# Kernel tuning notes

Measured on AMD Instinct MI355X. Metric: run time of the kernel, lower is better.

Reference implementation:

```python
import jax, jax.numpy as jnp
import numpy as np

B, T, H, C = 16, 6000, 256, 105
NOTE_BD_TEMP = 1.0
THRESH = 0.5
MIN_GAP = 19      # round(100 * 24000 / 1000 / 128)
REF_GAP = 9       # round(50 * 24000 / 1000 / 128)


def setup_inputs() -> dict:
    key = jax.random.key(0)
    kf, kw = jax.random.split(key)
    feat = jax.random.normal(kf, (B, T, H), dtype=jnp.float32)
    # kaiming normal fan_in: std = sqrt(2/fan_in)
    W = jax.random.normal(kw, (C, H), dtype=jnp.float32) * np.float32(np.sqrt(2.0 / H))
    b = jnp.zeros((C,), dtype=jnp.float32)
    rng = np.random.default_rng(0)
    word_bd = np.zeros((B, T), dtype=np.int32)
    for i in range(B):
        pos = np.cumsum(rng.integers(25, 61, size=T // 25)) + 10
        pos = pos[pos < T - 2]
        word_bd[i, pos] = 1
    lengths = rng.integers(T // 2, T + 1, size=B)
    non_padding = (np.arange(T)[None, :] < lengths[:, None]).astype(np.float32)
    return {"feat": feat, "word_bd": jnp.asarray(word_bd),
            "non_padding": jnp.asarray(non_padding), "W": W, "b": b}


def _phase1(probs, bd):
    # Peak-picking + min-gap merging scan over one sequence.
    # probs, bd: [T]. Returns res: [T+1] int32 (slot T is a dummy write sink).
    def step(carry, inp):
        res, last, start, rmv, rmi = carry
        j, bj, pj = inp
        in_run = start >= 0
        upd = (~in_run) | (pj > rmv)          # running first-argmax of current run
        fin = (~bj) & in_run                  # run just ended at j
        bd_idx = rmi                          # argmax index of the run (== start if len 1)
        merge = fin & (bd_idx - last < MIN_GAP) & (last > 0)
        mid = jnp.round((bd_idx + last).astype(jnp.float32) / 2.0).astype(jnp.int32)
        bd_idx = jnp.where(merge, mid, bd_idx)
        res = res.at[jnp.where(merge, last, T)].set(0)
        res = res.at[jnp.where(fin, bd_idx, T)].set(1)
        last = jnp.where(fin, bd_idx, last)
        start = jnp.where(bj, jnp.where(in_run, start, j), jnp.where(fin, -1, start))
        rmv = jnp.where(bj & upd, pj, rmv)
        rmi = jnp.where(bj & upd, j, rmi)
        return (res, last, start, rmv, rmi), None

    init = (jnp.zeros((T + 1,), jnp.int32), jnp.int32(-1), jnp.int32(-1),
            jnp.float32(-1e30), jnp.int32(0))
    xs = (jnp.arange(T, dtype=jnp.int32), bd, probs)
    (res, _, _, _, _), _ = jax.lax.scan(step, init, xs)
    return res


def _phase2(res, ref):
    # Reconcile predicted boundaries with reference word boundaries.
    ds = jnp.arange(-REF_GAP, REF_GAP)        # window [j-g, j+g-1] == torch slice [j-g : j+g]
    ks = jnp.arange(1, REF_GAP + 1)

    def step(res, j):
        active = ref[j] == 1
        widx = j + ds
        valid = (widx >= 0) & (widx < T)
        cwidx = jnp.clip(widx, 0, T - 1)
        seg = jnp.sum(jnp.where(valid, res[cwidx], 0))
        b0 = seg == 0
        b1 = (seg == 1) & (res[j] != 1)
        b2 = seg > 1
        # branch seg>1: first (in l1,r1,l2,r2,... order) offending boundary to suppress
        lidx = jnp.maximum(0, j - ks)
        ridx = jnp.minimum(T - 1, j + ks)
        cl = (res[lidx] == 1) & (ref[lidx] != 1)
        cr = (res[ridx] == 1) & (ref[ridx] != 1)
        conds = jnp.stack([cl, cr], axis=1).reshape(-1)
        cands = jnp.stack([lidx, ridx], axis=1).reshape(-1)
        zidx = jnp.where(jnp.any(conds), cands[jnp.argmax(conds)], T)
        # apply branch effects (inactive writes go to dummy slot T)
        res = res.at[jnp.where(active & b1 & valid, widx, T)].set(ref[cwidx])
        res = res.at[jnp.where(active & b2, zidx, T)].set(0)
        res = res.at[jnp.where(active & (b0 | b2), j, T)].set(1)
        return res, None

    res, _ = jax.lax.scan(step, res, jnp.arange(T, dtype=jnp.int32))
    return res


def regulate_boundary(bd_logits, word_bd, non_padding):
    probs = jax.nn.sigmoid(bd_logits)
    bd = probs > THRESH
    res = jax.vmap(_phase1)(probs, bd)
    res = jax.vmap(_phase2)(res, word_bd)
    res = res[:, :T]                      # drop dummy slot
    res = res.at[:, 0].set(0)
    L = jnp.sum(non_padding, axis=1).astype(jnp.int32)   # [B]
    keep = jnp.arange(T)[None, :] < (L[:, None] - 1)     # zero out res[i, L-1:]
    return jnp.where(keep, res, 0)


def reference(feat, word_bd, non_padding, W, b):
    # note_head: Linear(H -> C); eval mode so dropout is identity
    logits = jnp.einsum('bth,ch->btc', feat, W) + b           # [B,T,C]
    note_bd_logits = jnp.clip(logits[:, :, 0] / NOTE_BD_TEMP, -16.0, 16.0)
    note_frame_logits = logits[:, :, 1:] / NOTE_BD_TEMP
    note_bd_pred = regulate_boundary(note_bd_logits, word_bd, non_padding)
    return note_bd_logits, note_frame_logits, note_bd_pred
```

## Files before the change

kernel.cpp:

```cpp
#include <hip/hip_runtime.h>

#define NB 16
#define TT 6000
#define HH 256
#define CC 105
#define MIN_GAP_ 19
#define REF_GAP_ 9

using short8  = __attribute__((ext_vector_type(8))) short;
using short4v = __attribute__((ext_vector_type(4))) short;
using f32x4   = __attribute__((ext_vector_type(4))) float;

static __device__ __forceinline__ short f2bf(float x) {
  unsigned u = __builtin_bit_cast(unsigned, x);
  unsigned r = (u + 0x7FFFu + ((u >> 16) & 1u)) >> 16;
  return (short)r;
}

__global__ __launch_bounds__(256) void wconv_kernel(
    const float* __restrict__ W, unsigned short* __restrict__ Wb) {
  const int idx = blockIdx.x * 256 + threadIdx.x;
  const int c = idx >> 8, k = idx & 255;
  const float v = (c < CC - 1) ? W[(size_t)(c + 1) * HH + k] : 0.f;
  Wb[idx] = (unsigned short)f2bf(v);
}

#define BMR 128

__global__ __launch_bounds__(512, 4) void gemm_mfma(
    const float* __restrict__ feat, const float* __restrict__ W,
    const float* __restrict__ bias, const unsigned short* __restrict__ Wb,
    float* __restrict__ out0, float* __restrict__ out1) {
  __shared__ __align__(16) unsigned short aS[BMR * 256];
  const int tid  = threadIdx.x;
  const int wid  = tid >> 6;
  const int lane = tid & 63;
  const int rl   = lane & 15;
  const int kg   = lane >> 4;
  const int row0 = blockIdx.x * BMR;

  float4 areg[16];
  {
    const float* fbase = feat + (size_t)(row0 + wid) * HH + lane * 4;
#pragma unroll
    for (int p = 0; p < 16; p++)
      areg[p] = *reinterpret_cast<const float4*>(fbase + (size_t)p * 8 * HH);
  }

  short8 breg[8];
  if (wid < 7) {
    const unsigned short* wbbase = Wb + ((size_t)(wid * 16 + rl) << 8) + kg * 8;
#pragma unroll
    for (int ks = 0; ks < 8; ks++)
      breg[ks] = *reinterpret_cast<const short8*>(wbbase + ks * 32);
  }

  const float4 w0 = *reinterpret_cast<const float4*>(W + lane * 4);
  const float b0 = bias[0];
#pragma unroll
  for (int p = 0; p < 16; p++) {
    const int lrow = p * 8 + wid;
    const float4 a = areg[p];
    float s = a.x * w0.x;
    s = fmaf(a.y, w0.y, s); s = fmaf(a.z, w0.z, s); s = fmaf(a.w, w0.w, s);
#pragma unroll
    for (int off = 1; off < 64; off <<= 1) s += __shfl_xor(s, off);
    if (lane == 0)
      out0[row0 + lrow] = fminf(fmaxf(s + b0, -16.f), 16.f);
    short4v bf;
    bf[0] = f2bf(a.x); bf[1] = f2bf(a.y); bf[2] = f2bf(a.z); bf[3] = f2bf(a.w);
    const int dst = (lrow << 9) + ((lane * 8) ^ ((lrow & 7) << 4));
    *reinterpret_cast<short4v*>((char*)aS + dst) = bf;
  }
  __syncthreads();

  if (wid < 7) {
    const int xr = (rl & 7) << 4;
    f32x4 acc[8];
#pragma unroll
    for (int rg = 0; rg < 8; rg++) acc[rg] = (f32x4){0.f, 0.f, 0.f, 0.f};

#pragma unroll
    for (int ks = 0; ks < 8; ks++) {
      const int slot = (ks * 64 + kg * 16) ^ xr;
#pragma unroll
      for (int rg = 0; rg < 8; rg++) {
        const short8 av = *reinterpret_cast<const short8*>(
            (const char*)aS + (((rg * 16 + rl) << 9) + slot));
        acc[rg] = __builtin_amdgcn_mfma_f32_16x16x32_bf16(av, breg[ks], acc[rg], 0, 0, 0);
      }
    }

    const int c = wid * 16 + rl;
    if (c < CC - 1) {
      const float bb = bias[c + 1];
#pragma unroll
      for (int rg = 0; rg < 8; rg++) {
        const int rbase = row0 + rg * 16 + kg * 4;
#pragma unroll
        for (int r = 0; r < 4; r++)
          out1[(size_t)(rbase + r) * (CC - 1) + c] = acc[rg][r] + bb;
      }
    }
  }
}

#define NW 192
#define NW_LAST 187
#define CHUNK 32
#define NCLS 19
#define MAXRUNS 3072
#define MAXCH 96

__global__ __launch_bounds__(512) void phase_kernel(
    const float* __restrict__ bd_logits,
    const int* __restrict__ word_bd,
    const float* __restrict__ non_padding,
    float* __restrict__ out2) {
  __shared__ __align__(16) float lbuf[TT];
  __shared__ unsigned char wbuf[TT];
  __shared__ int res[TT];
  __shared__ unsigned bdbits[NW];
  __shared__ int runIdx[MAXRUNS];
  __shared__ int outLast[MAXCH][NCLS + 1];
  __shared__ int chP0[MAXCH];
  __shared__ int inL[MAXCH + 1];
  __shared__ int wsum[8];
  __shared__ int wbase[8];
  __shared__ int L_sh, nruns_sh;

  const int b = blockIdx.x;
  const int tid = threadIdx.x;
  const int lane = tid & 63;
  const int wid = tid >> 6;
  if (tid == 0) L_sh = 0;
  __syncthreads();

  int cnt_np = 0;
#pragma unroll
  for (int k = 0; k < 12; k++) {
    const int j = k * 512 + tid;
    bool pred = false;
    if (j < TT) {
      const float l = bd_logits[(size_t)b * TT + j];
      lbuf[j] = l;
      pred = l > 0.f;
      wbuf[j] = (unsigned char)word_bd[(size_t)b * TT + j];
      res[j] = 0;
      cnt_np += (non_padding[(size_t)b * TT + j] != 0.f) ? 1 : 0;
    }
    const unsigned long long m = __ballot(pred);
    if (lane == 0) {
      const int w0 = (k * 512 + (tid & ~63)) >> 5;
      bdbits[w0]     = (unsigned)m;
      bdbits[w0 + 1] = (unsigned)(m >> 32);
    }
  }
#pragma unroll
  for (int off = 32; off; off >>= 1) cnt_np += __shfl_xor(cnt_np, off);
  if (lane == 0) atomicAdd(&L_sh, cnt_np);
  __syncthreads();

  int cnt = 0;
  unsigned ends = 0;
  if (tid < NW) {
    const unsigned cur = bdbits[tid];
    const unsigned pb = tid ? (bdbits[tid - 1] >> 31) : 0u;
    ends = ((cur << 1) | pb) & ~cur;
    if (tid == NW_LAST) ends &= 0xFFFFu;
    cnt = __popc(ends);
  }
  int v = cnt;
#pragma unroll
  for (int off = 1; off < 64; off <<= 1) {
    const int t = __shfl_up(v, off);
    if (lane >= off) v += t;
  }
  if (lane == 63) wsum[wid] = v;
  __syncthreads();
  if (tid == 0) {
    int s = 0;
#pragma unroll
    for (int w = 0; w < 8; w++) { wbase[w] = s; s += wsum[w]; }
    nruns_sh = s;
  }
  __syncthreads();
  int slot = wbase[wid] + v - cnt;

  if (ends) {
    unsigned m = ends;
    while (m) {
      const int bit = __builtin_ctz(m);
      m &= m - 1;
      const int e = tid * 32 + bit;
      const int eb = e - 1;
      int w = eb >> 5;
      const int bb = eb & 31;
      const unsigned z = bdbits[w] << (31 - bb);
      const unsigned nz = ~z;
      int run = nz ? __builtin_clz(nz) : 32;
      if (run == bb + 1) {
        while (w > 0) {
          w--;
          const unsigned nx = ~bdbits[w];
          const int t2 = nx ? __builtin_clz(nx) : 32;
          run += t2;
          if (t2 < 32) break;
        }
      }
      const int s = e - run;
      float mv = lbuf[s];
      int mi = s;
      for (int i = s + 1; i < e; i++) {
        const float val = lbuf[i];
        if (val > mv) { mv = val; mi = i; }
      }
      runIdx[slot++] = mi;
    }
  }
  __syncthreads();

  const int n = nruns_sh;
  const int nch = (n + CHUNK - 1) / CHUNK;
  for (int f = tid; f < nch * NCLS; f += 512) {
    const int ch = f / NCLS;
    const int cls = f - ch * NCLS;
    const int s = ch * CHUNK;
    const int e = (s + CHUNK < n) ? s + CHUNK : n;
    const int p0 = runIdx[s];
    if (cls == NCLS - 1) chP0[ch] = p0;
    int last = (cls < 18) ? (p0 - 18 + cls) : -1;
    for (int i = s; i < e; i++) {
      int bd = runIdx[i];
      if (last > 0 && bd - last < MIN_GAP_) {
        const int sum = bd + last;
        const int h = sum >> 1;
        bd = (sum & 1) ? (h + (h & 1)) : h;
      }
      last = bd;
    }
    outLast[ch][cls] = last;
  }
  __syncthreads();

  if (wid == 0) {
    int q = -1;
    int row = (lane < NCLS && nch > 0) ? outLast[0][lane] : -1;
    for (int ch = 0; ch < nch; ch++) {
      const int rown = (lane < NCLS && ch + 1 < nch) ? outLast[ch + 1][lane] : -1;
      const int p0 = chP0[ch];
      const int cls = (q > 0 && p0 - q < MIN_GAP_) ? (q - (p0 - 18)) : (NCLS - 1);
      if (lane == 0) inL[ch] = q;
      q = __shfl(row, cls);
      row = rown;
    }
    if (lane == 0) inL[nch] = q;
  }
  __syncthreads();

  for (int ch = tid; ch < nch; ch += 512) {
    const int s = ch * CHUNK;
    const int e = (s + CHUNK < n) ? s + CHUNK : n;
    const int qin = inL[ch];
    const int qout = inL[ch + 1];
    if (qin >= 0 && qin != qout) res[qin] = 1;
    int last = qin;
    for (int i = s; i < e; i++) {
      int bd = runIdx[i];
      if (last > 0 && bd - last < MIN_GAP_) {
        const int sum = bd + last;
        const int h = sum >> 1;
        bd = (sum & 1) ? (h + (h & 1)) : h;
        if (last != qout) res[last] = 0;
      }
      if (bd != qout) res[bd] = 1;
      last = bd;
    }
  }
  if (tid == 0 && n > 0) res[inL[nch]] = 1;
  __syncthreads();

  for (int j = tid; j < TT; j += 512) {
    if (wbuf[j] != 1) continue;
    const int lo = (j - REF_GAP_ < 0) ? 0 : j - REF_GAP_;
    const int hi = (j + REF_GAP_ - 1 > TT - 1) ? TT - 1 : j + REF_GAP_ - 1;
    int seg = 0;
    for (int w = lo; w <= hi; w++) seg += res[w];
    if (seg == 0) {
      res[j] = 1;
    } else if (seg == 1) {
      if (res[j] != 1) {
        for (int w = lo; w <= hi; w++) res[w] = (int)wbuf[w];
      }
    } else {
      int zidx = -1;
      for (int k = 1; k <= REF_GAP_; k++) {
        const int li = (j - k < 0) ? 0 : j - k;
        const int ri = (j + k > TT - 1) ? TT - 1 : j + k;
        if (res[li] == 1 && wbuf[li] != 1) { zidx = li; break; }
        if (res[ri] == 1 && wbuf[ri] != 1) { zidx = ri; break; }
      }
      if (zidx >= 0) res[zidx] = 0;
      res[j] = 1;
    }
  }
  __syncthreads();

  const int L = L_sh;
  for (int t = tid; t < TT; t += 512)
    out2[(size_t)b * TT + t] = (t >= 1 && t < L - 1) ? (float)res[t] : 0.f;
}

extern "C" void kernel_launch(void* const* d_in, const int* in_sizes, int n_in,
                              void* d_out, int out_size, void* d_ws, size_t ws_size,
                              hipStream_t stream) {
  const float* feat        = (const float*)d_in[0];
  const int*   word_bd     = (const int*)d_in[1];
  const float* non_padding = (const float*)d_in[2];
  const float* W           = (const float*)d_in[3];
  const float* bias        = (const float*)d_in[4];

  float* out  = (float*)d_out;
  float* out0 = out;
  float* out1 = out + (size_t)NB * TT;
  float* out2 = out + (size_t)NB * TT + (size_t)NB * TT * (CC - 1);

  unsigned short* Wb = (unsigned short*)d_ws;

  hipLaunchKernelGGL(wconv_kernel, dim3(112), dim3(256), 0, stream, W, Wb);
  hipLaunchKernelGGL(gemm_mfma, dim3((NB * TT) / BMR), dim3(512), 0, stream,
                     feat, W, bias, Wb, out0, out1);
  hipLaunchKernelGGL(phase_kernel, dim3(NB), dim3(512), 0, stream,
                     out0, word_bd, non_padding, out2);
}
```

Before: 73.99 us.

## Make GEMM blocks persistent over three 64-row tiles with double-buffered LDS

The GEMM now launches 500 blocks, each handling three 64-row tiles instead of one 128-row tile per block. LDS is double-buffered, and the global feature loads for the next tile are issued before the MFMA and store work on the current tile. The aim is to hide global load latency behind compute and to reuse the B-fragment registers across tiles. In exchange there are fewer blocks, so parallelism drops, and register pressure may rise.

```diff
diff --git a/kernel.cpp b/kernel.cpp
--- a/kernel.cpp
+++ b/kernel.cpp
@@ -25,27 +25,21 @@
   Wb[idx] = (unsigned short)f2bf(v);
 }
 
-#define BMR 128
+#define BMT 64
+#define TPB 3
+#define NGB 500
 
 __global__ __launch_bounds__(512, 4) void gemm_mfma(
     const float* __restrict__ feat, const float* __restrict__ W,
     const float* __restrict__ bias, const unsigned short* __restrict__ Wb,
     float* __restrict__ out0, float* __restrict__ out1) {
-  __shared__ __align__(16) unsigned short aS[BMR * 256];
+  __shared__ __align__(16) unsigned short aS[2][BMT * 256];
   const int tid  = threadIdx.x;
   const int wid  = tid >> 6;
   const int lane = tid & 63;
   const int rl   = lane & 15;
   const int kg   = lane >> 4;
-  const int row0 = blockIdx.x * BMR;
-
-  float4 areg[16];
-  {
-    const float* fbase = feat + (size_t)(row0 + wid) * HH + lane * 4;
-#pragma unroll
-    for (int p = 0; p < 16; p++)
-      areg[p] = *reinterpret_cast<const float4*>(fbase + (size_t)p * 8 * HH);
-  }
+  const int brow0 = blockIdx.x * (BMT * TPB);
 
   short8 breg[8];
   if (wid < 7) {
@@ -57,50 +51,75 @@
 
   const float4 w0 = *reinterpret_cast<const float4*>(W + lane * 4);
   const float b0 = bias[0];
-#pragma unroll
-  for (int p = 0; p < 16; p++) {
-    const int lrow = p * 8 + wid;
-    const float4 a = areg[p];
-    float s = a.x * w0.x;
-    s = fmaf(a.y, w0.y, s); s = fmaf(a.z, w0.z, s); s = fmaf(a.w, w0.w, s);
-#pragma unroll
-    for (int off = 1; off < 64; off <<= 1) s += __shfl_xor(s, off);
-    if (lane == 0)
-      out0[row0 + lrow] = fminf(fmaxf(s + b0, -16.f), 16.f);
-    short4v bf;
-    bf[0] = f2bf(a.x); bf[1] = f2bf(a.y); bf[2] = f2bf(a.z); bf[3] = f2bf(a.w);
-    const int dst = (lrow << 9) + ((lane * 8) ^ ((lrow & 7) << 4));
-    *reinterpret_cast<short4v*>((char*)aS + dst) = bf;
-  }
-  __syncthreads();
-
-  if (wid < 7) {
-    const int xr = (rl & 7) << 4;
-    f32x4 acc[8];
-#pragma unroll
-    for (int rg = 0; rg < 8; rg++) acc[rg] = (f32x4){0.f, 0.f, 0.f, 0.f};
-
-#pragma unroll
-    for (int ks = 0; ks < 8; ks++) {
-      const int slot = (ks * 64 + kg * 16) ^ xr;
-#pragma unroll
-      for (int rg = 0; rg < 8; rg++) {
-        const short8 av = *reinterpret_cast<const short8*>(
-            (const char*)aS + (((rg * 16 + rl) << 9) + slot));
-        acc[rg] = __builtin_amdgcn_mfma_f32_16x16x32_bf16(av, breg[ks], acc[rg], 0, 0, 0);
-      }
-    }
-
-    const int c = wid * 16 + rl;
-    if (c < CC - 1) {
-      const float bb = bias[c + 1];
-#pragma unroll
-      for (int rg = 0; rg < 8; rg++) {
-        const int rbase = row0 + rg * 16 + kg * 4;
-#pragma unroll
-        for (int r = 0; r < 4; r++)
-          out1[(size_t)(rbase + r) * (CC - 1) + c] = acc[rg][r] + bb;
-      }
+  const int cch = wid * 16 + rl;
+  const float bb = (wid < 7 && cch < CC - 1) ? bias[cch + 1] : 0.f;
+  const int xr = (rl & 7) << 4;
+
+  float4 areg[8];
+
+  auto loadA = [&](int trow0) {
+    const float* fbase = feat + (size_t)(trow0 + wid) * HH + lane * 4;
+#pragma unroll
+    for (int q = 0; q < 8; q++)
+      areg[q] = *reinterpret_cast<const float4*>(fbase + (size_t)q * 8 * HH);
+  };
+
+  auto stage = [&](int buf, int trow0) {
+#pragma unroll
+    for (int q = 0; q < 8; q++) {
+      const int lrow = q * 8 + wid;
+      const float4 a = areg[q];
+      float s = a.x * w0.x;
+      s = fmaf(a.y, w0.y, s); s = fmaf(a.z, w0.z, s); s = fmaf(a.w, w0.w, s);
+#pragma unroll
+      for (int off = 1; off < 64; off <<= 1) s += __shfl_xor(s, off);
+      if (lane == 0)
+        out0[trow0 + lrow] = fminf(fmaxf(s + b0, -16.f), 16.f);
+      short4v bf;
+      bf[0] = f2bf(a.x); bf[1] = f2bf(a.y); bf[2] = f2bf(a.z); bf[3] = f2bf(a.w);
+      const int dst = (lrow << 9) + ((lane * 8) ^ ((lrow & 7) << 4));
+      *reinterpret_cast<short4v*>((char*)aS[buf] + dst) = bf;
+    }
+  };
+
+  auto mfmaStore = [&](int buf, int trow0) {
+    if (wid < 7) {
+      f32x4 acc[4];
+#pragma unroll
+      for (int rg = 0; rg < 4; rg++) acc[rg] = (f32x4){0.f, 0.f, 0.f, 0.f};
+#pragma unroll
+      for (int ks = 0; ks < 8; ks++) {
+        const int slot = (ks * 64 + kg * 16) ^ xr;
+#pragma unroll
+        for (int rg = 0; rg < 4; rg++) {
+          const short8 av = *reinterpret_cast<const short8*>(
+              (const char*)aS[buf] + (((rg * 16 + rl) << 9) + slot));
+          acc[rg] = __builtin_amdgcn_mfma_f32_16x16x32_bf16(av, breg[ks], acc[rg], 0, 0, 0);
+        }
+      }
+      if (cch < CC - 1) {
+#pragma unroll
+        for (int rg = 0; rg < 4; rg++) {
+          const int rbase = trow0 + rg * 16 + kg * 4;
+#pragma unroll
+          for (int r = 0; r < 4; r++)
+            out1[(size_t)(rbase + r) * (CC - 1) + cch] = acc[rg][r] + bb;
+        }
+      }
+    }
+  };
+
+  loadA(brow0);
+  stage(0, brow0);
+  __syncthreads();
+
+#pragma unroll
+  for (int t = 0; t < TPB; t++) {
+    if (t + 1 < TPB) loadA(brow0 + (t + 1) * BMT);
+    mfmaStore(t & 1, brow0 + t * BMT);
+    if (t + 1 < TPB) {
+      stage((t + 1) & 1, brow0 + (t + 1) * BMT);
+      __syncthreads();
     }
   }
 }
@@ -328,7 +347,7 @@
   unsigned short* Wb = (unsigned short*)d_ws;
 
   hipLaunchKernelGGL(wconv_kernel, dim3(112), dim3(256), 0, stream, W, Wb);
-  hipLaunchKernelGGL(gemm_mfma, dim3((NB * TT) / BMR), dim3(512), 0, stream,
+  hipLaunchKernelGGL(gemm_mfma, dim3(NGB), dim3(512), 0, stream,
                      feat, W, bias, Wb, out0, out1);
   hipLaunchKernelGGL(phase_kernel, dim3(NB), dim3(512), 0, stream,
                      out0, word_bd, non_padding, out2);
```

New measurement: 77.16 us. 4.3% more time.
